# Kernel optimization log

Measured on AMD Instinct MI355X. Metric: run time of the kernel, lower is better.

## Reference

```python
import jax, jax.numpy as jnp
import numpy as np

NODE_DIM = 32
NUM_NODES = 256
BATCH = 32
HIDDEN = 64


def setup_inputs() -> dict:
    key = jax.random.key(0)
    k1, k2, k3, k4, k5 = jax.random.split(key, 5)
    node_features = jax.random.normal(k1, (BATCH, NUM_NODES, NODE_DIM), dtype=jnp.float32)
    # nn.Linear(node_dim*2, 64): weight [64, 2*node_dim], bias [64]
    s1 = 1.0 / np.sqrt(2 * NODE_DIM)
    W1 = jax.random.uniform(k2, (HIDDEN, 2 * NODE_DIM), minval=-s1, maxval=s1, dtype=jnp.float32)
    b1 = jax.random.uniform(k3, (HIDDEN,), minval=-s1, maxval=s1, dtype=jnp.float32)
    # nn.Linear(64, 1): weight [1, 64], bias [1]
    s2 = 1.0 / np.sqrt(HIDDEN)
    W2 = jax.random.uniform(k4, (1, HIDDEN), minval=-s2, maxval=s2, dtype=jnp.float32)
    b2 = jax.random.uniform(k5, (1,), minval=-s2, maxval=s2, dtype=jnp.float32)
    return {"node_features": node_features, "W1": W1, "b1": b1, "W2": W2, "b2": b2}


def reference(node_features, W1, b1, W2, b2):
    # fc1(concat(x_i, x_j)) splits as x_i @ W1a^T + x_j @ W1b^T (exact same math,
    # avoids materializing the [B,N,N,2d] pair tensor).
    d = node_features.shape[-1]
    W1a, W1b = W1[:, :d], W1[:, d:]
    Ai = jnp.einsum('bnd,hd->bnh', node_features, W1a)  # [B,N,H]
    Aj = jnp.einsum('bnd,hd->bnh', node_features, W1b)  # [B,N,H]
    hidden = jax.nn.relu(Ai[:, :, None, :] + Aj[:, None, :, :] + b1)  # [B,N,N,H]
    logits = jnp.einsum('bijh,h->bij', hidden, W2[0]) + b2[0]  # [B,N,N]
    return jax.nn.sigmoid(logits)
```

## Files before the change

kernel.cpp:

```cpp
#include <hip/hip_runtime.h>

typedef _Float16 h2 __attribute__((ext_vector_type(2)));
typedef _Float16 h8 __attribute__((ext_vector_type(8)));

#define BB 32
#define NN 256
#define DD 32
#define HH 64
#define ETI 128
#define ETJ 64
#define XST 40
#define AST 72

#if defined(__has_builtin)
#  if __has_builtin(__builtin_amdgcn_fdot2)
#    define FDOT2(a, b, c) __builtin_amdgcn_fdot2((a), (b), (c), false)
#  endif
#endif
#ifndef FDOT2
#  define FDOT2(a, b, c) ((c) + (float)((a)[0]) * (float)((b)[0]) + (float)((a)[1]) * (float)((b)[1]))
#endif

__device__ __forceinline__ float sigmoidf_fast(float v) {
    return 1.0f / (1.0f + __expf(-v));
}

__global__ __launch_bounds__(256) void fused_kernel(const float* __restrict__ x, const float* __restrict__ W1,
                                                    const float* __restrict__ b1, const float* __restrict__ W2,
                                                    const float* __restrict__ b2, float* __restrict__ out)
{
    __shared__ _Float16 sX[192][XST];
    __shared__ _Float16 sW[128][XST];
    __shared__ _Float16 sAi[ETI][AST];
    __shared__ _Float16 sAj[ETJ][AST];
    __shared__ _Float16 sW2h[HH];
    __shared__ float sb1[HH];

    const int blk = blockIdx.x;
    const int jt = blk & 3;
    const int it = (blk >> 2) & 1;
    const int b  = blk >> 3;
    const int tid = threadIdx.x;
    const float* xb = x + (size_t)b * NN * DD;

    {
        const int hc = tid >> 1, d0 = (tid & 1) << 4;
        const float* src = (hc < HH) ? &W1[hc * 64 + d0] : &W1[(hc - HH) * 64 + DD + d0];
        float t16[16];
        *(float4*)&t16[0]  = *(const float4*)&src[0];
        *(float4*)&t16[4]  = *(const float4*)&src[4];
        *(float4*)&t16[8]  = *(const float4*)&src[8];
        *(float4*)&t16[12] = *(const float4*)&src[12];
        const int phys = (hc >> 3) + ((hc & 7) << 4);
        h8 v0, v1;
#pragma unroll
        for (int q = 0; q < 8; ++q) { v0[q] = (_Float16)t16[q]; v1[q] = (_Float16)t16[q + 8]; }
        *(h8*)&sW[phys][d0]     = v0;
        *(h8*)&sW[phys][d0 + 8] = v1;
    }
    for (int k = tid; k < 384; k += 256) {
        const int row = k >> 1, d0 = (k & 1) << 4;
        int grow, phys;
        if (row < 128) { grow = it * ETI + row; phys = (row >> 3) + ((row & 7) << 4); }
        else { const int r = row - 128; grow = jt * ETJ + r; phys = 128 + (r >> 2) + ((r & 3) << 4); }
        float t16[16];
        const float* src = &xb[(size_t)grow * DD + d0];
        *(float4*)&t16[0]  = *(const float4*)&src[0];
        *(float4*)&t16[4]  = *(const float4*)&src[4];
        *(float4*)&t16[8]  = *(const float4*)&src[8];
        *(float4*)&t16[12] = *(const float4*)&src[12];
        h8 v0, v1;
#pragma unroll
        for (int q = 0; q < 8; ++q) { v0[q] = (_Float16)t16[q]; v1[q] = (_Float16)t16[q + 8]; }
        *(h8*)&sX[phys][d0]     = v0;
        *(h8*)&sX[phys][d0 + 8] = v1;
    }
    if (tid < HH) sW2h[tid] = (_Float16)W2[tid];
    else if (tid < 2 * HH) sb1[tid - HH] = b1[tid - HH];
    __syncthreads();

    {
        const int wid = tid >> 6, lane = tid & 63;
        const int lq = lane >> 3, lp = lane & 7;
        if (wid < 2) {
            const int q = (wid << 3) | lq;
            float pacc[8][8] = {};
#pragma unroll
            for (int ch = 0; ch < 4; ++ch) {
                h8 xv[8], wv[8];
#pragma unroll
                for (int rr = 0; rr < 8; ++rr) xv[rr] = *(const h8*)&sX[q + (rr << 4)][ch << 3];
#pragma unroll
                for (int cc = 0; cc < 8; ++cc) wv[cc] = *(const h8*)&sW[lp + (cc << 4)][ch << 3];
#pragma unroll
                for (int rr = 0; rr < 8; ++rr)
#pragma unroll
                    for (int cc = 0; cc < 8; ++cc) {
                        float a = pacc[rr][cc];
                        a = FDOT2(__builtin_shufflevector(xv[rr], xv[rr], 0, 1), __builtin_shufflevector(wv[cc], wv[cc], 0, 1), a);
                        a = FDOT2(__builtin_shufflevector(xv[rr], xv[rr], 2, 3), __builtin_shufflevector(wv[cc], wv[cc], 2, 3), a);
                        a = FDOT2(__builtin_shufflevector(xv[rr], xv[rr], 4, 5), __builtin_shufflevector(wv[cc], wv[cc], 4, 5), a);
                        a = FDOT2(__builtin_shufflevector(xv[rr], xv[rr], 6, 7), __builtin_shufflevector(wv[cc], wv[cc], 6, 7), a);
                        pacc[rr][cc] = a;
                    }
            }
#pragma unroll
            for (int rr = 0; rr < 8; ++rr) {
                h8 v;
#pragma unroll
                for (int cc = 0; cc < 8; ++cc) v[cc] = (_Float16)pacc[rr][cc];
                *(h8*)&sAi[(q << 3) | rr][lp << 3] = v;
            }
        } else {
            const int wp = wid - 2;
            float pacc[4][8] = {};
#pragma unroll
            for (int ch = 0; ch < 4; ++ch) {
                h8 xv[4], wv[8];
#pragma unroll
                for (int rr = 0; rr < 4; ++rr) xv[rr] = *(const h8*)&sX[128 + (wp << 3) + lq + (rr << 4)][ch << 3];
#pragma unroll
                for (int cc = 0; cc < 8; ++cc) wv[cc] = *(const h8*)&sW[8 + lp + (cc << 4)][ch << 3];
#pragma unroll
                for (int rr = 0; rr < 4; ++rr)
#pragma unroll
                    for (int cc = 0; cc < 8; ++cc) {
                        float a = pacc[rr][cc];
                        a = FDOT2(__builtin_shufflevector(xv[rr], xv[rr], 0, 1), __builtin_shufflevector(wv[cc], wv[cc], 0, 1), a);
                        a = FDOT2(__builtin_shufflevector(xv[rr], xv[rr], 2, 3), __builtin_shufflevector(wv[cc], wv[cc], 2, 3), a);
                        a = FDOT2(__builtin_shufflevector(xv[rr], xv[rr], 4, 5), __builtin_shufflevector(wv[cc], wv[cc], 4, 5), a);
                        a = FDOT2(__builtin_shufflevector(xv[rr], xv[rr], 6, 7), __builtin_shufflevector(wv[cc], wv[cc], 6, 7), a);
                        pacc[rr][cc] = a;
                    }
            }
#pragma unroll
            for (int rr = 0; rr < 4; ++rr) {
                h8 v;
#pragma unroll
                for (int cc = 0; cc < 8; ++cc) v[cc] = (_Float16)(pacc[rr][cc] + sb1[(lp << 3) + cc]);
                *(h8*)&sAj[(wp << 5) + (lq << 2) + rr][lp << 3] = v;
            }
        }
    }
    __syncthreads();

    const int jl = tid & 15;
    const int il = tid >> 4;
    h8 w2v[8];
#pragma unroll
    for (int q = 0; q < 8; ++q) w2v[q] = *(const h8*)&sW2h[q << 3];

    float eacc[8][4] = {};
#pragma unroll
    for (int c8 = 0; c8 < 8; ++c8) {
        h8 av[8], cv[4];
#pragma unroll
        for (int r = 0; r < 8; ++r) av[r] = *(const h8*)&sAi[il + (r << 4)][c8 << 3];
#pragma unroll
        for (int c = 0; c < 4; ++c) cv[c] = *(const h8*)&sAj[jl + (c << 4)][c8 << 3];
#pragma unroll
        for (int r = 0; r < 8; ++r)
#pragma unroll
            for (int c = 0; c < 4; ++c) {
                h8 z  = av[r] + cv[c];
                h8 rl = __builtin_elementwise_max(z, h8{});
                float a = eacc[r][c];
                a = FDOT2(__builtin_shufflevector(rl, rl, 0, 1), __builtin_shufflevector(w2v[c8], w2v[c8], 0, 1), a);
                a = FDOT2(__builtin_shufflevector(rl, rl, 2, 3), __builtin_shufflevector(w2v[c8], w2v[c8], 2, 3), a);
                a = FDOT2(__builtin_shufflevector(rl, rl, 4, 5), __builtin_shufflevector(w2v[c8], w2v[c8], 4, 5), a);
                a = FDOT2(__builtin_shufflevector(rl, rl, 6, 7), __builtin_shufflevector(w2v[c8], w2v[c8], 6, 7), a);
                eacc[r][c] = a;
            }
    }

    const float b2v = b2[0];
    const size_t base = (((size_t)(b * NN) + it * ETI + il) << 8) + jt * ETJ + jl;
#pragma unroll
    for (int r = 0; r < 8; ++r)
#pragma unroll
        for (int c = 0; c < 4; ++c)
            out[base + (size_t)(r << 4) * NN + (c << 4)] = sigmoidf_fast(eacc[r][c] + b2v);
}

extern "C" void kernel_launch(void* const* d_in, const int* in_sizes, int n_in,
                              void* d_out, int out_size, void* d_ws, size_t ws_size,
                              hipStream_t stream) {
    const float* x  = (const float*)d_in[0];
    const float* W1 = (const float*)d_in[1];
    const float* b1 = (const float*)d_in[2];
    const float* W2 = (const float*)d_in[3];
    const float* b2 = (const float*)d_in[4];
    float* out = (float*)d_out;

    const int nBlocks = BB * (NN / ETI) * (NN / ETJ);
    fused_kernel<<<nBlocks, 256, 0, stream>>>(x, W1, b1, W2, b2, out);
}
```

Baseline: 17.99 us.

## Double threads per block to 512 and split per-thread work in half

Launches 512 threads per block instead of 256 and redistributes every phase: W1 staging, x staging, and both projection GEMMs (4 waves compute Ai, 4 compute Aj), plus halving the per-thread output tile in the pairwise stage from 8x4 to 4x4. Shared-memory row permutations are changed to match. The goal is more waves per block to hide latency and to cut per-thread register use and serial work. The cost is more threads sharing the same small smem tiles, with more redundant W2 and W1 loads per output.

```diff
diff --git a/kernel.cpp b/kernel.cpp
--- a/kernel.cpp
+++ b/kernel.cpp
@@ -25,7 +25,7 @@
     return 1.0f / (1.0f + __expf(-v));
 }
 
-__global__ __launch_bounds__(256) void fused_kernel(const float* __restrict__ x, const float* __restrict__ W1,
+__global__ __launch_bounds__(512) void fused_kernel(const float* __restrict__ x, const float* __restrict__ W1,
                                                     const float* __restrict__ b1, const float* __restrict__ W2,
                                                     const float* __restrict__ b2, float* __restrict__ out)
 {
@@ -44,25 +44,22 @@
     const float* xb = x + (size_t)b * NN * DD;
 
     {
-        const int hc = tid >> 1, d0 = (tid & 1) << 4;
+        const int hc = tid >> 2, d0 = (tid & 3) << 3;
         const float* src = (hc < HH) ? &W1[hc * 64 + d0] : &W1[(hc - HH) * 64 + DD + d0];
-        float t16[16];
-        *(float4*)&t16[0]  = *(const float4*)&src[0];
-        *(float4*)&t16[4]  = *(const float4*)&src[4];
-        *(float4*)&t16[8]  = *(const float4*)&src[8];
-        *(float4*)&t16[12] = *(const float4*)&src[12];
+        float t8[8];
+        *(float4*)&t8[0] = *(const float4*)&src[0];
+        *(float4*)&t8[4] = *(const float4*)&src[4];
         const int phys = (hc >> 3) + ((hc & 7) << 4);
-        h8 v0, v1;
+        h8 v;
 #pragma unroll
-        for (int q = 0; q < 8; ++q) { v0[q] = (_Float16)t16[q]; v1[q] = (_Float16)t16[q + 8]; }
-        *(h8*)&sW[phys][d0]     = v0;
-        *(h8*)&sW[phys][d0 + 8] = v1;
+        for (int q = 0; q < 8; ++q) v[q] = (_Float16)t8[q];
+        *(h8*)&sW[phys][d0] = v;
     }
-    for (int k = tid; k < 384; k += 256) {
-        const int row = k >> 1, d0 = (k & 1) << 4;
+    if (tid < 384) {
+        const int row = tid >> 1, d0 = (tid & 1) << 4;
         int grow, phys;
-        if (row < 128) { grow = it * ETI + row; phys = (row >> 3) + ((row & 7) << 4); }
-        else { const int r = row - 128; grow = jt * ETJ + r; phys = 128 + (r >> 2) + ((r & 3) << 4); }
+        if (row < 128) { grow = it * ETI + row; phys = (row >> 2) + ((row & 3) << 5); }
+        else { const int r = row - 128; grow = jt * ETJ + r; phys = 128 + (r >> 1) + ((r & 1) << 5); }
         float t16[16];
         const float* src = &xb[(size_t)grow * DD + d0];
         *(float4*)&t16[0]  = *(const float4*)&src[0];
@@ -82,45 +79,16 @@
     {
         const int wid = tid >> 6, lane = tid & 63;
         const int lq = lane >> 3, lp = lane & 7;
-        if (wid < 2) {
-            const int q = (wid << 3) | lq;
-            float pacc[8][8] = {};
-#pragma unroll
-            for (int ch = 0; ch < 4; ++ch) {
-                h8 xv[8], wv[8];
-#pragma unroll
-                for (int rr = 0; rr < 8; ++rr) xv[rr] = *(const h8*)&sX[q + (rr << 4)][ch << 3];
-#pragma unroll
-                for (int cc = 0; cc < 8; ++cc) wv[cc] = *(const h8*)&sW[lp + (cc << 4)][ch << 3];
-#pragma unroll
-                for (int rr = 0; rr < 8; ++rr)
-#pragma unroll
-                    for (int cc = 0; cc < 8; ++cc) {
-                        float a = pacc[rr][cc];
-                        a = FDOT2(__builtin_shufflevector(xv[rr], xv[rr], 0, 1), __builtin_shufflevector(wv[cc], wv[cc], 0, 1), a);
-                        a = FDOT2(__builtin_shufflevector(xv[rr], xv[rr], 2, 3), __builtin_shufflevector(wv[cc], wv[cc], 2, 3), a);
-                        a = FDOT2(__builtin_shufflevector(xv[rr], xv[rr], 4, 5), __builtin_shufflevector(wv[cc], wv[cc], 4, 5), a);
-                        a = FDOT2(__builtin_shufflevector(xv[rr], xv[rr], 6, 7), __builtin_shufflevector(wv[cc], wv[cc], 6, 7), a);
-                        pacc[rr][cc] = a;
-                    }
-            }
-#pragma unroll
-            for (int rr = 0; rr < 8; ++rr) {
-                h8 v;
-#pragma unroll
-                for (int cc = 0; cc < 8; ++cc) v[cc] = (_Float16)pacc[rr][cc];
-                *(h8*)&sAi[(q << 3) | rr][lp << 3] = v;
-            }
-        } else {
-            const int wp = wid - 2;
+        if (wid < 4) {
+            const int g = (wid << 3) | lq;
             float pacc[4][8] = {};
 #pragma unroll
             for (int ch = 0; ch < 4; ++ch) {
                 h8 xv[4], wv[8];
 #pragma unroll
-                for (int rr = 0; rr < 4; ++rr) xv[rr] = *(const h8*)&sX[128 + (wp << 3) + lq + (rr << 4)][ch << 3];
+                for (int rr = 0; rr < 4; ++rr) xv[rr] = *(const h8*)&sX[g + (rr << 5)][ch << 3];
 #pragma unroll
-                for (int cc = 0; cc < 8; ++cc) wv[cc] = *(const h8*)&sW[8 + lp + (cc << 4)][ch << 3];
+                for (int cc = 0; cc < 8; ++cc) wv[cc] = *(const h8*)&sW[lp + (cc << 4)][ch << 3];
 #pragma unroll
                 for (int rr = 0; rr < 4; ++rr)
 #pragma unroll
@@ -137,8 +105,37 @@
             for (int rr = 0; rr < 4; ++rr) {
                 h8 v;
 #pragma unroll
+                for (int cc = 0; cc < 8; ++cc) v[cc] = (_Float16)pacc[rr][cc];
+                *(h8*)&sAi[(g << 2) | rr][lp << 3] = v;
+            }
+        } else {
+            const int g = ((wid - 4) << 3) | lq;
+            float pacc[2][8] = {};
+#pragma unroll
+            for (int ch = 0; ch < 4; ++ch) {
+                h8 xv[2], wv[8];
+#pragma unroll
+                for (int rr = 0; rr < 2; ++rr) xv[rr] = *(const h8*)&sX[128 + g + (rr << 5)][ch << 3];
+#pragma unroll
+                for (int cc = 0; cc < 8; ++cc) wv[cc] = *(const h8*)&sW[8 + lp + (cc << 4)][ch << 3];
+#pragma unroll
+                for (int rr = 0; rr < 2; ++rr)
+#pragma unroll
+                    for (int cc = 0; cc < 8; ++cc) {
+                        float a = pacc[rr][cc];
+                        a = FDOT2(__builtin_shufflevector(xv[rr], xv[rr], 0, 1), __builtin_shufflevector(wv[cc], wv[cc], 0, 1), a);
+                        a = FDOT2(__builtin_shufflevector(xv[rr], xv[rr], 2, 3), __builtin_shufflevector(wv[cc], wv[cc], 2, 3), a);
+                        a = FDOT2(__builtin_shufflevector(xv[rr], xv[rr], 4, 5), __builtin_shufflevector(wv[cc], wv[cc], 4, 5), a);
+                        a = FDOT2(__builtin_shufflevector(xv[rr], xv[rr], 6, 7), __builtin_shufflevector(wv[cc], wv[cc], 6, 7), a);
+                        pacc[rr][cc] = a;
+                    }
+            }
+#pragma unroll
+            for (int rr = 0; rr < 2; ++rr) {
+                h8 v;
+#pragma unroll
                 for (int cc = 0; cc < 8; ++cc) v[cc] = (_Float16)(pacc[rr][cc] + sb1[(lp << 3) + cc]);
-                *(h8*)&sAj[(wp << 5) + (lq << 2) + rr][lp << 3] = v;
+                *(h8*)&sAj[(g << 1) | rr][lp << 3] = v;
             }
         }
     }
@@ -150,16 +147,16 @@
 #pragma unroll
     for (int q = 0; q < 8; ++q) w2v[q] = *(const h8*)&sW2h[q << 3];
 
-    float eacc[8][4] = {};
+    float eacc[4][4] = {};
 #pragma unroll
     for (int c8 = 0; c8 < 8; ++c8) {
-        h8 av[8], cv[4];
+        h8 av[4], cv[4];
 #pragma unroll
-        for (int r = 0; r < 8; ++r) av[r] = *(const h8*)&sAi[il + (r << 4)][c8 << 3];
+        for (int r = 0; r < 4; ++r) av[r] = *(const h8*)&sAi[il + (r << 5)][c8 << 3];
 #pragma unroll
         for (int c = 0; c < 4; ++c) cv[c] = *(const h8*)&sAj[jl + (c << 4)][c8 << 3];
 #pragma unroll
-        for (int r = 0; r < 8; ++r)
+        for (int r = 0; r < 4; ++r)
 #pragma unroll
             for (int c = 0; c < 4; ++c) {
                 h8 z  = av[r] + cv[c];
@@ -176,10 +173,10 @@
     const float b2v = b2[0];
     const size_t base = (((size_t)(b * NN) + it * ETI + il) << 8) + jt * ETJ + jl;
 #pragma unroll
-    for (int r = 0; r < 8; ++r)
+    for (int r = 0; r < 4; ++r)
 #pragma unroll
         for (int c = 0; c < 4; ++c)
-            out[base + (size_t)(r << 4) * NN + (c << 4)] = sigmoidf_fast(eacc[r][c] + b2v);
+            out[base + (size_t)(r << 5) * NN + (c << 4)] = sigmoidf_fast(eacc[r][c] + b2v);
 }
 
 extern "C" void kernel_launch(void* const* d_in, const int* in_sizes, int n_in,
@@ -193,5 +190,5 @@
     float* out = (float*)d_out;
 
     const int nBlocks = BB * (NN / ETI) * (NN / ETJ);
-    fused_kernel<<<nBlocks, 256, 0, stream>>>(x, W1, b1, W2, b2, out);
+    fused_kernel<<<nBlocks, 512, 0, stream>>>(x, W1, b1, W2, b2, out);
 }
```

Result: faster. 16.98 us (median of 2 runs) (-5.6%).
